# Kernel tuning notes

Hardware: AMD Instinct MI355X
Metric: run time of the kernel (lower is better)

The kernel has to match this reference:

```python
import jax, jax.numpy as jnp
import numpy as np

B, S, D, R = 8, 2048, 2048, 256


def soft_threshold24(w):
    """2:4 soft-threshold: in each contiguous group of 4 along the last dim,
    keep the top-2 |w| and shrink them by the 3rd-largest |w| (soft threshold),
    zeroing the bottom two. Mirrors soft_threshold24_triton."""
    rows, K = w.shape
    g = w.reshape(rows, K // 4, 4)
    a = jnp.abs(g)
    t = jnp.sort(a, axis=-1)[..., 1:2]  # 2nd smallest == 3rd largest per group
    sp = jnp.sign(g) * jnp.maximum(a - t, 0.0)
    return sp.reshape(rows, K)


def fp16_mm(a, b):
    """fake_fp8_mm: cast operands to fp16, matmul with fp32 accumulation/output."""
    return jnp.matmul(a.astype(jnp.float16), b.astype(jnp.float16),
                      preferred_element_type=jnp.float32)


def sparse_linear(x, w, b, scale):
    """SparseOverlayFunction.forward: 2:4-sparsified, scaled weight + fp16 GEMM."""
    x2 = x.reshape(-1, x.shape[-1])                # [N, K]
    ws = soft_threshold24(w) * scale               # [K, M], 2:4 sparse * learnable scale
    out = fp16_mm(x2, ws)                          # [N, M] fp32
    out = out.reshape(x.shape[:-1] + (w.shape[-1],))
    return out + b


def setup_inputs():
    key = jax.random.key(0)
    ks = jax.random.split(key, 4)
    x = jax.random.normal(ks[0], (B, S, D), jnp.float32)
    weight_in = jax.random.normal(ks[1], (D, R), jnp.float32) * 0.02
    weight_out = jax.random.normal(ks[2], (R, D), jnp.float32) * 0.02
    bias_in = jnp.zeros((R,), jnp.float32)
    bias_out = jax.random.normal(ks[3], (D,), jnp.float32) * 0.01
    sparse_scale_in = jnp.ones((1,), jnp.float32)
    sparse_scale_out = jnp.ones((1,), jnp.float32)
    return {"x": x, "weight_in": weight_in, "weight_out": weight_out,
            "bias_in": bias_in, "bias_out": bias_out,
            "sparse_scale_in": sparse_scale_in, "sparse_scale_out": sparse_scale_out}


def reference(x, weight_in, weight_out, bias_in, bias_out, sparse_scale_in, sparse_scale_out):
    h = sparse_linear(x, weight_in, bias_in, sparse_scale_in)    # [B,S,R]
    y = sparse_linear(h, weight_out, bias_out, sparse_scale_out)  # [B,S,D]
    return y
```

## Files before the change

### kernel.cpp

```cpp
#include <hip/hip_runtime.h>
#include <stdint.h>
#include <stddef.h>

typedef _Float16 f16;
typedef __attribute__((ext_vector_type(8))) _Float16 f16x8;
typedef __attribute__((ext_vector_type(4))) float f32x4;

#define GPTR(p) ((const __attribute__((address_space(1))) void*)(p))
#define LPTR(p) ((__attribute__((address_space(3))) void*)(p))

__device__ __forceinline__ void async16(const void* g, void* l) {
    __builtin_amdgcn_global_load_lds(GPTR(g), LPTR(l), 16, 0, 0);
}

__global__ __launch_bounds__(256) void sparsify_t_tiled(
        const float* __restrict__ W, const float* __restrict__ scale,
        f16* __restrict__ Wt, int K, int M) {
    __shared__ f16 T[64][80];
    const int r0 = blockIdx.y << 6, m0 = blockIdx.x << 6;
    const float s = scale[0];
    const int t = threadIdx.x;
    const int rr = t >> 2, mb = (t & 3) << 4;
    const float* src = W + (size_t)(r0 + rr) * M + m0 + mb;
    #pragma unroll
    for (int j = 0; j < 4; j++) {
        float4 v = *(const float4*)(src + j * 4);
        float a0 = fabsf(v.x), a1 = fabsf(v.y), a2 = fabsf(v.z), a3 = fabsf(v.w);
        float lo1 = fminf(a0, a1), hi1 = fmaxf(a0, a1);
        float lo2 = fminf(a2, a3), hi2 = fmaxf(a2, a3);
        float th = fminf(fmaxf(lo1, lo2), fminf(hi1, hi2));
        int m = mb + j * 4;
        T[m + 0][rr] = (f16)(copysignf(fmaxf(a0 - th, 0.f), v.x) * s);
        T[m + 1][rr] = (f16)(copysignf(fmaxf(a1 - th, 0.f), v.y) * s);
        T[m + 2][rr] = (f16)(copysignf(fmaxf(a2 - th, 0.f), v.z) * s);
        T[m + 3][rr] = (f16)(copysignf(fmaxf(a3 - th, 0.f), v.w) * s);
    }
    __syncthreads();
    const int mm = t >> 2, rb = (t & 3) << 4;
    f16* dst = Wt + (size_t)(m0 + mm) * K + r0 + rb;
    *(f16x8*)dst       = *(const f16x8*)&T[mm][rb];
    *(f16x8*)(dst + 8) = *(const f16x8*)&T[mm][rb + 8];
}

__global__ __launch_bounds__(256, 4) void gemm1_kernel(
        const float* __restrict__ A, const f16* __restrict__ Bt,
        const float* __restrict__ bias, f16* __restrict__ H) {
    constexpr int K = 2048, RN = 256, BK = 64;
    __shared__ float4 Asf[64 * 16];
    __shared__ f16x8  Bs[64 * 8];

    const int tid  = threadIdx.x;
    const int lane = tid & 63;
    const int wv   = tid >> 6;
    const int wm   = wv & 1, wn = wv >> 1;
    const int lr   = lane & 15, q = lane >> 4;
    const int row0 = blockIdx.y << 6;
    const int col0 = blockIdx.x << 6;

    f32x4 acc[2][2] = {};

    for (int k0 = 0; k0 < K; k0 += BK) {
        #pragma unroll
        for (int j = 0; j < 4; j++) {
            int issue = wv * 4 + j;
            int L = issue * 64 + lane;
            int r = L >> 4, cp = L & 15;
            int c = (cp & 8) | ((cp & 7) ^ (r & 7));
            async16(A + (size_t)(row0 + r) * K + k0 + c * 4,
                    (char*)Asf + issue * 1024);
        }
        #pragma unroll
        for (int j = 0; j < 2; j++) {
            int issue = wv * 2 + j;
            int L = issue * 64 + lane;
            int r = L >> 3, cp = L & 7;
            int c = cp ^ (r & 7);
            async16(Bt + (size_t)(col0 + r) * K + k0 + c * 8,
                    (char*)Bs + issue * 1024);
        }
        __syncthreads();

        #pragma unroll
        for (int ks = 0; ks < 2; ks++) {
            f16x8 af[2], bf[2];
            #pragma unroll
            for (int m = 0; m < 2; m++) {
                int r = wm * 32 + m * 16 + lr;
                int c0p = ks * 8 + (((2 * q) + 0) ^ (r & 7));
                int c1p = ks * 8 + (((2 * q) + 1) ^ (r & 7));
                float4 v0 = Asf[r * 16 + c0p];
                float4 v1 = Asf[r * 16 + c1p];
                f16x8 h;
                h[0] = (f16)v0.x; h[1] = (f16)v0.y; h[2] = (f16)v0.z; h[3] = (f16)v0.w;
                h[4] = (f16)v1.x; h[5] = (f16)v1.y; h[6] = (f16)v1.z; h[7] = (f16)v1.w;
                af[m] = h;
            }
            #pragma unroll
            for (int n = 0; n < 2; n++) {
                int r = wn * 32 + n * 16 + lr;
                int cp = (ks * 4 + q) ^ (r & 7);
                bf[n] = Bs[r * 8 + cp];
            }
            #pragma unroll
            for (int m = 0; m < 2; m++)
                #pragma unroll
                for (int n = 0; n < 2; n++)
                    acc[m][n] = __builtin_amdgcn_mfma_f32_16x16x32_f16(
                        af[m], bf[n], acc[m][n], 0, 0, 0);
        }
        __syncthreads();
    }

    #pragma unroll
    for (int m = 0; m < 2; m++) {
        int gr0 = row0 + wm * 32 + m * 16 + q * 4;
        #pragma unroll
        for (int n = 0; n < 2; n++) {
            int gc = col0 + wn * 32 + n * 16 + lr;
            float bv = bias[gc];
            #pragma unroll
            for (int r = 0; r < 4; r++)
                H[(size_t)(gr0 + r) * RN + gc] = (f16)(acc[m][n][r] + bv);
        }
    }
}

__global__ __launch_bounds__(256, 4) void gemm2_kernel(
        const f16* __restrict__ H, const f16* __restrict__ Bt,
        const float* __restrict__ bias, float* __restrict__ Y) {
    constexpr int K = 256, N = 2048, BK = 64;
    __shared__ f16x8 As[64 * 8];
    __shared__ f16x8 Bs[128 * 8];

    const int tid  = threadIdx.x;
    const int lane = tid & 63;
    const int wv   = tid >> 6;
    const int wm   = wv & 1, wn = wv >> 1;
    const int lr   = lane & 15, q = lane >> 4;
    const int row0 = blockIdx.y << 6;
    const int col0 = blockIdx.x << 7;

    f32x4 acc[2][4] = {};

    for (int k0 = 0; k0 < K; k0 += BK) {
        #pragma unroll
        for (int j = 0; j < 2; j++) {
            int issue = wv * 2 + j;
            int L = issue * 64 + lane;
            int r = L >> 3, cp = L & 7;
            int c = cp ^ (r & 7);
            async16(H + (size_t)(row0 + r) * K + k0 + c * 8,
                    (char*)As + issue * 1024);
        }
        #pragma unroll
        for (int j = 0; j < 4; j++) {
            int issue = wv * 4 + j;
            int L = issue * 64 + lane;
            int r = L >> 3, cp = L & 7;
            int c = cp ^ (r & 7);
            async16(Bt + (size_t)(col0 + r) * K + k0 + c * 8,
                    (char*)Bs + issue * 1024);
        }
        __syncthreads();

        #pragma unroll
        for (int ks = 0; ks < 2; ks++) {
            f16x8 af[2], bf[4];
            #pragma unroll
            for (int m = 0; m < 2; m++) {
                int r = wm * 32 + m * 16 + lr;
                af[m] = As[r * 8 + ((ks * 4 + q) ^ (r & 7))];
            }
            #pragma unroll
            for (int n = 0; n < 4; n++) {
                int r = wn * 64 + n * 16 + lr;
                bf[n] = Bs[r * 8 + ((ks * 4 + q) ^ (r & 7))];
            }
            #pragma unroll
            for (int m = 0; m < 2; m++)
                #pragma unroll
                for (int n = 0; n < 4; n++)
                    acc[m][n] = __builtin_amdgcn_mfma_f32_16x16x32_f16(
                        af[m], bf[n], acc[m][n], 0, 0, 0);
        }
        __syncthreads();
    }

    #pragma unroll
    for (int m = 0; m < 2; m++) {
        int gr0 = row0 + wm * 32 + m * 16 + q * 4;
        #pragma unroll
        for (int n = 0; n < 4; n++) {
            int gc = col0 + wn * 64 + n * 16 + lr;
            float bv = bias[gc];
            #pragma unroll
            for (int r = 0; r < 4; r++)
                Y[(size_t)(gr0 + r) * N + gc] = acc[m][n][r] + bv;
        }
    }
}

extern "C" void kernel_launch(void* const* d_in, const int* in_sizes, int n_in,
                              void* d_out, int out_size, void* d_ws, size_t ws_size,
                              hipStream_t stream) {
    const float* x  = (const float*)d_in[0];
    const float* w1 = (const float*)d_in[1];
    const float* w2 = (const float*)d_in[2];
    const float* b1 = (const float*)d_in[3];
    const float* b2 = (const float*)d_in[4];
    const float* s1 = (const float*)d_in[5];
    const float* s2 = (const float*)d_in[6];
    float* y = (float*)d_out;

    constexpr int NROWS = 8 * 2048;
    constexpr int D = 2048, R = 256;

    char* ws = (char*)d_ws;
    f16* W1t = (f16*)ws;
    f16* W2t = (f16*)(ws + (size_t)R * D * 2);
    f16* H   = (f16*)(ws + (size_t)R * D * 4);

    hipLaunchKernelGGL(sparsify_t_tiled, dim3(R / 64, D / 64), dim3(256),
                       0, stream, w1, s1, W1t, D, R);
    hipLaunchKernelGGL(sparsify_t_tiled, dim3(D / 64, R / 64), dim3(256),
                       0, stream, w2, s2, W2t, R, D);

    hipLaunchKernelGGL(gemm1_kernel, dim3(R / 64, NROWS / 64), dim3(256),
                       0, stream, x, W1t, b1, H);

    hipLaunchKernelGGL(gemm2_kernel, dim3(D / 128, NROWS / 64), dim3(256),
                       0, stream, H, W2t, b2, y);
}
```

Before: 297.7 us.

## Shrink GEMM tiles, raise occupancy, and remap blocks with XCD-aware swizzle

Both GEMMs get smaller block tiles: gemm1 drops from 64x64 to 32x64 rows and gemm2 from 64x128 to 64x64. The grids become 1-D with an XCD-aware mapping so that the blocks landing on each XCD share rows of A. Launch bounds rise to 8 blocks per CU to hide load latency, since the loop has no double buffering. The cost is less operand reuse per block, which means more global and LDS traffic per output element.

```diff
diff --git a/kernel.cpp b/kernel.cpp
--- a/kernel.cpp
+++ b/kernel.cpp
@@ -42,41 +42,111 @@
     *(f16x8*)(dst + 8) = *(const f16x8*)&T[mm][rb + 8];
 }
 
-__global__ __launch_bounds__(256, 4) void gemm1_kernel(
+__global__ __launch_bounds__(256, 8) void gemm1_kernel(
         const float* __restrict__ A, const f16* __restrict__ Bt,
         const float* __restrict__ bias, f16* __restrict__ H) {
     constexpr int K = 2048, RN = 256, BK = 64;
-    __shared__ float4 Asf[64 * 16];
+    __shared__ float4 Asf[32 * 16];
     __shared__ f16x8  Bs[64 * 8];
+
+    const int f = blockIdx.x;
+    const int xcd = f & 7, j = f >> 3;
+    const int row0 = (xcd + ((j >> 2) << 3)) << 5;
+    const int col0 = (j & 3) << 6;
 
     const int tid  = threadIdx.x;
     const int lane = tid & 63;
     const int wv   = tid >> 6;
     const int wm   = wv & 1, wn = wv >> 1;
     const int lr   = lane & 15, q = lane >> 4;
-    const int row0 = blockIdx.y << 6;
-    const int col0 = blockIdx.x << 6;
+
+    f32x4 acc[2] = {};
+
+    for (int k0 = 0; k0 < K; k0 += BK) {
+        #pragma unroll
+        for (int jj = 0; jj < 2; jj++) {
+            int issue = wv * 2 + jj;
+            int L = issue * 64 + lane;
+            int r = L >> 4, p = L & 15;
+            int c = (p & 8) | ((p & 7) ^ (r & 7));
+            async16(A + (size_t)(row0 + r) * K + k0 + c * 4, &Asf[issue * 64]);
+        }
+        #pragma unroll
+        for (int jj = 0; jj < 2; jj++) {
+            int issue = wv * 2 + jj;
+            int L = issue * 64 + lane;
+            int r = L >> 3, p = L & 7;
+            int c = p ^ (r & 7);
+            async16(Bt + (size_t)(col0 + r) * K + k0 + c * 8, &Bs[issue * 64]);
+        }
+        __syncthreads();
+
+        #pragma unroll
+        for (int ks = 0; ks < 2; ks++) {
+            int ar = wm * 16 + lr;
+            int c0 = ks * 8 + 2 * q, c1 = c0 + 1;
+            float4 v0 = Asf[ar * 16 + ((c0 & 8) | ((c0 & 7) ^ (ar & 7)))];
+            float4 v1 = Asf[ar * 16 + ((c1 & 8) | ((c1 & 7) ^ (ar & 7)))];
+            f16x8 af;
+            af[0] = (f16)v0.x; af[1] = (f16)v0.y; af[2] = (f16)v0.z; af[3] = (f16)v0.w;
+            af[4] = (f16)v1.x; af[5] = (f16)v1.y; af[6] = (f16)v1.z; af[7] = (f16)v1.w;
+            #pragma unroll
+            for (int n = 0; n < 2; n++) {
+                int br = wn * 32 + n * 16 + lr;
+                f16x8 bf = Bs[br * 8 + ((ks * 4 + q) ^ (br & 7))];
+                acc[n] = __builtin_amdgcn_mfma_f32_16x16x32_f16(af, bf, acc[n], 0, 0, 0);
+            }
+        }
+        __syncthreads();
+    }
+
+    const int gr0 = row0 + wm * 16 + q * 4;
+    #pragma unroll
+    for (int n = 0; n < 2; n++) {
+        int gc = col0 + wn * 32 + n * 16 + lr;
+        float bv = bias[gc];
+        #pragma unroll
+        for (int r = 0; r < 4; r++)
+            H[(size_t)(gr0 + r) * RN + gc] = (f16)(acc[n][r] + bv);
+    }
+}
+
+__global__ __launch_bounds__(256, 8) void gemm2_kernel(
+        const f16* __restrict__ H, const f16* __restrict__ Bt,
+        const float* __restrict__ bias, float* __restrict__ Y) {
+    constexpr int K = 256, N = 2048, BK = 64;
+    __shared__ f16x8 As[64 * 8];
+    __shared__ f16x8 Bs[64 * 8];
+
+    const int f = blockIdx.x;
+    const int xcd = f & 7, j = f >> 3;
+    const int row0 = (xcd + ((j >> 5) << 3)) << 6;
+    const int col0 = (j & 31) << 6;
+
+    const int tid  = threadIdx.x;
+    const int lane = tid & 63;
+    const int wv   = tid >> 6;
+    const int wm   = wv & 1, wn = wv >> 1;
+    const int lr   = lane & 15, q = lane >> 4;
 
     f32x4 acc[2][2] = {};
 
     for (int k0 = 0; k0 < K; k0 += BK) {
         #pragma unroll
-        for (int j = 0; j < 4; j++) {
-            int issue = wv * 4 + j;
-            int L = issue * 64 + lane;
-            int r = L >> 4, cp = L & 15;
-            int c = (cp & 8) | ((cp & 7) ^ (r & 7));
-            async16(A + (size_t)(row0 + r) * K + k0 + c * 4,
-                    (char*)Asf + issue * 1024);
-        }
-        #pragma unroll
-        for (int j = 0; j < 2; j++) {
-            int issue = wv * 2 + j;
-            int L = issue * 64 + lane;
-            int r = L >> 3, cp = L & 7;
-            int c = cp ^ (r & 7);
-            async16(Bt + (size_t)(col0 + r) * K + k0 + c * 8,
-                    (char*)Bs + issue * 1024);
+        for (int jj = 0; jj < 2; jj++) {
+            int issue = wv * 2 + jj;
+            int L = issue * 64 + lane;
+            int r = L >> 3, p = L & 7;
+            int c = p ^ (r & 7);
+            async16(H + (size_t)(row0 + r) * K + k0 + c * 8, &As[issue * 64]);
+        }
+        #pragma unroll
+        for (int jj = 0; jj < 2; jj++) {
+            int issue = wv * 2 + jj;
+            int L = issue * 64 + lane;
+            int r = L >> 3, p = L & 7;
+            int c = p ^ (r & 7);
+            async16(Bt + (size_t)(col0 + r) * K + k0 + c * 8, &Bs[issue * 64]);
         }
         __syncthreads();
 
@@ -86,20 +156,12 @@
             #pragma unroll
             for (int m = 0; m < 2; m++) {
                 int r = wm * 32 + m * 16 + lr;
-                int c0p = ks * 8 + (((2 * q) + 0) ^ (r & 7));
-                int c1p = ks * 8 + (((2 * q) + 1) ^ (r & 7));
-                float4 v0 = Asf[r * 16 + c0p];
-                float4 v1 = Asf[r * 16 + c1p];
-                f16x8 h;
-                h[0] = (f16)v0.x; h[1] = (f16)v0.y; h[2] = (f16)v0.z; h[3] = (f16)v0.w;
-                h[4] = (f16)v1.x; h[5] = (f16)v1.y; h[6] = (f16)v1.z; h[7] = (f16)v1.w;
-                af[m] = h;
+                af[m] = As[r * 8 + ((ks * 4 + q) ^ (r & 7))];
             }
             #pragma unroll
             for (int n = 0; n < 2; n++) {
                 int r = wn * 32 + n * 16 + lr;
-                int cp = (ks * 4 + q) ^ (r & 7);
-                bf[n] = Bs[r * 8 + cp];
+                bf[n] = Bs[r * 8 + ((ks * 4 + q) ^ (r & 7))];
             }
             #pragma unroll
             for (int m = 0; m < 2; m++)
@@ -117,81 +179,6 @@
         #pragma unroll
         for (int n = 0; n < 2; n++) {
             int gc = col0 + wn * 32 + n * 16 + lr;
-            float bv = bias[gc];
-            #pragma unroll
-            for (int r = 0; r < 4; r++)
-                H[(size_t)(gr0 + r) * RN + gc] = (f16)(acc[m][n][r] + bv);
-        }
-    }
-}
-
-__global__ __launch_bounds__(256, 4) void gemm2_kernel(
-        const f16* __restrict__ H, const f16* __restrict__ Bt,
-        const float* __restrict__ bias, float* __restrict__ Y) {
-    constexpr int K = 256, N = 2048, BK = 64;
-    __shared__ f16x8 As[64 * 8];
-    __shared__ f16x8 Bs[128 * 8];
-
-    const int tid  = threadIdx.x;
-    const int lane = tid & 63;
-    const int wv   = tid >> 6;
-    const int wm   = wv & 1, wn = wv >> 1;
-    const int lr   = lane & 15, q = lane >> 4;
-    const int row0 = blockIdx.y << 6;
-    const int col0 = blockIdx.x << 7;
-
-    f32x4 acc[2][4] = {};
-
-    for (int k0 = 0; k0 < K; k0 += BK) {
-        #pragma unroll
-        for (int j = 0; j < 2; j++) {
-            int issue = wv * 2 + j;
-            int L = issue * 64 + lane;
-            int r = L >> 3, cp = L & 7;
-            int c = cp ^ (r & 7);
-            async16(H + (size_t)(row0 + r) * K + k0 + c * 8,
-                    (char*)As + issue * 1024);
-        }
-        #pragma unroll
-        for (int j = 0; j < 4; j++) {
-            int issue = wv * 4 + j;
-            int L = issue * 64 + lane;
-            int r = L >> 3, cp = L & 7;
-            int c = cp ^ (r & 7);
-            async16(Bt + (size_t)(col0 + r) * K + k0 + c * 8,
-                    (char*)Bs + issue * 1024);
-        }
-        __syncthreads();
-
-        #pragma unroll
-        for (int ks = 0; ks < 2; ks++) {
-            f16x8 af[2], bf[4];
-            #pragma unroll
-            for (int m = 0; m < 2; m++) {
-                int r = wm * 32 + m * 16 + lr;
-                af[m] = As[r * 8 + ((ks * 4 + q) ^ (r & 7))];
-            }
-            #pragma unroll
-            for (int n = 0; n < 4; n++) {
-                int r = wn * 64 + n * 16 + lr;
-                bf[n] = Bs[r * 8 + ((ks * 4 + q) ^ (r & 7))];
-            }
-            #pragma unroll
-            for (int m = 0; m < 2; m++)
-                #pragma unroll
-                for (int n = 0; n < 4; n++)
-                    acc[m][n] = __builtin_amdgcn_mfma_f32_16x16x32_f16(
-                        af[m], bf[n], acc[m][n], 0, 0, 0);
-        }
-        __syncthreads();
-    }
-
-    #pragma unroll
-    for (int m = 0; m < 2; m++) {
-        int gr0 = row0 + wm * 32 + m * 16 + q * 4;
-        #pragma unroll
-        for (int n = 0; n < 4; n++) {
-            int gc = col0 + wn * 64 + n * 16 + lr;
             float bv = bias[gc];
             #pragma unroll
             for (int r = 0; r < 4; r++)
@@ -225,9 +212,9 @@
     hipLaunchKernelGGL(sparsify_t_tiled, dim3(D / 64, R / 64), dim3(256),
                        0, stream, w2, s2, W2t, R, D);
 
-    hipLaunchKernelGGL(gemm1_kernel, dim3(R / 64, NROWS / 64), dim3(256),
-                       0, stream, x, W1t, b1, H);
-
-    hipLaunchKernelGGL(gemm2_kernel, dim3(D / 128, NROWS / 64), dim3(256),
-                       0, stream, H, W2t, b2, y);
-}
+    hipLaunchKernelGGL(gemm1_kernel, dim3(2048), dim3(256), 0, stream,
+                       x, W1t, b1, H);
+
+    hipLaunchKernelGGL(gemm2_kernel, dim3(8192), dim3(256), 0, stream,
+                       H, W2t, b2, y);
+}
```

Measured after the change: 300.4 us. No clear change (+0.9%).
